# Performance work log

Hardware: AMD Instinct MI355X
Metric: run time of the kernel (lower is better)

Reference implementation:

```python
import jax, jax.numpy as jnp
import numpy as np

BLOCK = 32          # per_1x32 microscaling block size along K
FP4_MAX = 6.0       # largest magnitude representable in e2m1
FP4_EMAX = 2.0      # exponent of largest fp4 binade (4..6)


def _quant_dequant_mxfp4(x):
    """Simulate MXFP4 (e2m1 elements, shared power-of-two E8M0 scale per 1x32
    block along the last dim): quantize then dequantize. x: [..., K], K % 32 == 0."""
    shape = x.shape
    xb = x.reshape(*shape[:-1], shape[-1] // BLOCK, BLOCK)
    amax = jnp.max(jnp.abs(xb), axis=-1, keepdims=True)
    # shared scale: 2^(floor(log2(amax)) - emax) so the block max lands in the top binade
    exp = jnp.floor(jnp.log2(jnp.maximum(amax, jnp.finfo(x.dtype).tiny))) - FP4_EMAX
    scale = jnp.where(amax > 0, jnp.exp2(exp), jnp.ones_like(amax))
    q = jnp.clip(xb / scale, -FP4_MAX, FP4_MAX)
    aq = jnp.abs(q)
    # e2m1 ulp: 0.5 on [0,2), 1 on [2,4), 2 on [4,6]
    lsb = jnp.where(aq < 2.0, 0.5, jnp.where(aq < 4.0, 1.0, 2.0))
    qr = jnp.round(q / lsb) * lsb  # round-to-nearest-even onto the fp4 grid
    return (qr * scale).reshape(shape)


def setup_inputs() -> dict:
    key = jax.random.key(0)
    k1, k2, k3 = jax.random.split(key, 3)
    B, S, K, N = 4, 2048, 2048, 2048
    inp = jax.random.normal(k1, (B, S, K), dtype=jnp.float32)
    weight = jax.random.normal(k2, (N, K), dtype=jnp.float32) * (1.0 / np.sqrt(K))
    bias = jax.random.normal(k3, (N,), dtype=jnp.float32) * 0.02
    return {"input": inp, "weight": weight, "bias": bias}


def reference(input, weight, bias):
    # both activation and weight are fake-quantized to MXFP4 per 1x32 blocks
    # along the contraction (in_features) dim, then a standard GEMM + bias.
    orig_shape = input.shape
    a = _quant_dequant_mxfp4(input.reshape(-1, orig_shape[-1]))  # [M, K]
    w = _quant_dequant_mxfp4(weight)                              # [N, K]
    out = jnp.einsum("mk,nk->mn", a, w) + bias
    return out.reshape(*orig_shape[:-1], weight.shape[0])
```

## Files before the change

### kernel.cpp

```cpp
#include <hip/hip_runtime.h>
#include <cstdint>


#define BM 256
#define BN 256
#define BK 256

typedef float floatx16 __attribute__((ext_vector_type(16)));
typedef int intx8 __attribute__((ext_vector_type(8)));

#define GLOBAL_AS __attribute__((address_space(1)))
#define LDS_AS __attribute__((address_space(3)))


__device__ __forceinline__ int enc1(float x, float inv) {
    float q = x * inv;
    q = fminf(fmaxf(q, -6.0f), 6.0f);
    int s = (int)(__float_as_uint(q) >> 31) << 3;
    float aq = fabsf(q);
    float ilsb = aq < 2.0f ? 2.0f : (aq < 4.0f ? 1.0f : 0.5f);
    float lsb  = aq < 2.0f ? 0.5f : (aq < 4.0f ? 1.0f : 2.0f);
    float ar = rintf(aq * ilsb) * lsb;
    int c;
    if (ar < 2.0f)      c = (int)(ar * 2.0f);
    else if (ar < 4.0f) c = 2 + (int)ar;
    else                c = 4 + (int)(ar * 0.5f);
    return c | s;
}

__global__ void quant_mxfp4_v5(const float* __restrict__ A, uint8_t* __restrict__ Aq,
                               uint8_t* __restrict__ Asc,
                               const float* __restrict__ W, uint8_t* __restrict__ Wq,
                               uint8_t* __restrict__ Wsc,
                               long na4, long ntot4, int s4, long Mr, long Nr) {
    long t = (long)blockIdx.x * 256 + threadIdx.x;
    if (t >= ntot4) return;
    const float* src; uint8_t* dq; uint8_t* ds; long idx; long rows;
    if (t < na4) { src = A; dq = Aq; ds = Asc; idx = t; rows = Mr; }
    else         { src = W; dq = Wq; ds = Wsc; idx = t - na4; rows = Nr; }

    float4 f = ((const float4*)src)[idx];
    float amax = fmaxf(fmaxf(fabsf(f.x), fabsf(f.y)),
                       fmaxf(fabsf(f.z), fabsf(f.w)));
    amax = fmaxf(amax, __shfl_xor(amax, 1));
    amax = fmaxf(amax, __shfl_xor(amax, 2));
    amax = fmaxf(amax, __shfl_xor(amax, 4));

    int ebits = (int)((__float_as_uint(amax) >> 23) & 0xff);
    int sb;
    float inv;
    if (amax > 0.0f) {
        sb = ebits - 2; if (sb < 0) sb = 0;
        inv = __uint_as_float((unsigned)((256 - ebits) & 255) << 23);
    } else {
        sb = 127;
        inv = 0.0f;
    }

    int c0 = enc1(f.x, inv), c1 = enc1(f.y, inv);
    int c2 = enc1(f.z, inv), c3 = enc1(f.w, inv);
    ((unsigned short*)dq)[idx] =
        (unsigned short)(c0 | (c1 << 4) | (c2 << 8) | (c3 << 12));
    if ((idx & 7) == 0) {
        long m  = idx >> s4;
        int  kb = (int)((idx & ((1L << s4) - 1)) >> 3);
        ds[((size_t)(kb >> 3) * rows + m) * 8 + (kb & 7)] = (uint8_t)sb;
    }
}


#define GITER(T, CUR, NXT)                                                     \
  {                                                                            \
    const int p_ = (T) & 1;                                                    \
    const uint8_t* pa_ = sA[p_];                                               \
    const uint8_t* pb_ = sB[p_];                                               \
    if ((T) + 1 < NT) {                                                        \
      _Pragma("unroll") for (int mi = 0; mi < 4; ++mi)                         \
        sgA[NXT][mi] = *(const uint2*)(Asc +                                   \
            ((size_t)((T) + 1) * M + m0 + rA0 + mi * 32) * 8);                 \
      _Pragma("unroll") for (int ni = 0; ni < 2; ++ni)                         \
        sgB[NXT][ni] = *(const uint2*)(Wsc +                                   \
            ((size_t)((T) + 1) * N + n0 + rB0 + ni * 32) * 8);                 \
    }                                                                          \
    __builtin_amdgcn_sched_barrier(0);                                         \
    int4 fa_[4], fb_[2];                                                       \
    _Pragma("unroll") for (int mi = 0; mi < 4; ++mi)                           \
      fa_[mi] = *(const int4*)(pa_ + (rA0 + mi * 32) * 128 + (q2 ^ swz) * 16); \
    _Pragma("unroll") for (int ni = 0; ni < 2; ++ni)                           \
      fb_[ni] = *(const int4*)(pb_ + (rB0 + ni * 32) * 128 + (q2 ^ swz) * 16); \
    __builtin_amdgcn_s_setprio(1);                                             \
    _Pragma("unroll") for (int ks = 0; ks < 4; ++ks) {                         \
      int4 na_[4], nb_[2];                                                     \
      if (ks < 3) {                                                            \
        const int off_ = (((ks + 1) * 2 + q2) ^ swz) * 16;                     \
        _Pragma("unroll") for (int mi = 0; mi < 4; ++mi)                       \
          na_[mi] = *(const int4*)(pa_ + (rA0 + mi * 32) * 128 + off_);        \
        _Pragma("unroll") for (int ni = 0; ni < 2; ++ni)                       \
          nb_[ni] = *(const int4*)(pb_ + (rB0 + ni * 32) * 128 + off_);        \
      }                                                                        \
      int sav_[4], sbv_[2];                                                    \
      _Pragma("unroll") for (int mi = 0; mi < 4; ++mi)                         \
        sav_[mi] = (int)(((ks < 2) ? (sgA[CUR][mi].x >> ((ks * 2 + q2) * 8))   \
                   : (sgA[CUR][mi].y >> (((ks - 2) * 2 + q2) * 8))) & 0xffu);  \
      _Pragma("unroll") for (int ni = 0; ni < 2; ++ni)                         \
        sbv_[ni] = (int)(((ks < 2) ? (sgB[CUR][ni].x >> ((ks * 2 + q2) * 8))   \
                   : (sgB[CUR][ni].y >> (((ks - 2) * 2 + q2) * 8))) & 0xffu);  \
      intx8 b80_, b81_;                                                        \
      b80_[0] = fb_[0].x; b80_[1] = fb_[0].y; b80_[2] = fb_[0].z;              \
      b80_[3] = fb_[0].w; b80_[4] = 0; b80_[5] = 0; b80_[6] = 0; b80_[7] = 0;  \
      b81_[0] = fb_[1].x; b81_[1] = fb_[1].y; b81_[2] = fb_[1].z;              \
      b81_[3] = fb_[1].w; b81_[4] = 0; b81_[5] = 0; b81_[6] = 0; b81_[7] = 0;  \
      _Pragma("unroll") for (int mi = 0; mi < 4; ++mi) {                       \
        intx8 a8_;                                                             \
        a8_[0] = fa_[mi].x; a8_[1] = fa_[mi].y; a8_[2] = fa_[mi].z;            \
        a8_[3] = fa_[mi].w; a8_[4] = 0; a8_[5] = 0; a8_[6] = 0; a8_[7] = 0;    \
        acc[mi][0] = __builtin_amdgcn_mfma_scale_f32_32x32x64_f8f6f4(          \
            a8_, b80_, acc[mi][0], 4, 4, 0, sav_[mi], 0, sbv_[0]);             \
        acc[mi][1] = __builtin_amdgcn_mfma_scale_f32_32x32x64_f8f6f4(          \
            a8_, b81_, acc[mi][1], 4, 4, 0, sav_[mi], 0, sbv_[1]);             \
      }                                                                        \
      if (ks < 3) {                                                            \
        _Pragma("unroll") for (int mi = 0; mi < 4; ++mi) fa_[mi] = na_[mi];    \
        _Pragma("unroll") for (int ni = 0; ni < 2; ++ni) fb_[ni] = nb_[ni];    \
      }                                                                        \
    }                                                                          \
    __builtin_amdgcn_s_setprio(0);                                             \
    if ((T) + 1 < NT) {                                                        \
      asm volatile("s_waitcnt lgkmcnt(0)" ::: "memory");                       \
      __builtin_amdgcn_sched_barrier(0);                                       \
      __builtin_amdgcn_s_barrier();                                            \
      if ((T) + 2 < NT) stage((T) + 2);                                        \
      __builtin_amdgcn_sched_barrier(0);                                       \
      if ((T) + 2 < NT) asm volatile("s_waitcnt vmcnt(8)" ::: "memory");       \
      else              asm volatile("s_waitcnt vmcnt(0)" ::: "memory");       \
      __builtin_amdgcn_sched_barrier(0);                                       \
      __builtin_amdgcn_s_barrier();                                            \
    }                                                                          \
  }

__global__ __launch_bounds__(512, 2) void gemm_fp4_v9(
        const uint8_t* __restrict__ Aq, const uint8_t* __restrict__ Asc,
        const uint8_t* __restrict__ Wq, const uint8_t* __restrict__ Wsc,
        const float* __restrict__ bias, float* __restrict__ C,
        int M, int N, int K) {
    __shared__ __align__(16) uint8_t sA[2][BM * 128];
    __shared__ __align__(16) uint8_t sB[2][BN * 128];

    const int tid = threadIdx.x;
    const int lane = tid & 63;
    const int w = tid >> 6;
    const int wr = w >> 2;
    const int wc = w & 3;
    const int row32 = lane & 31;
    const int q2 = lane >> 5;

    const int id = blockIdx.x;
    const int g = id & 7, h = id >> 3;
    const int by = g * 4 + (h & 3);
    const int bx = h >> 2;
    const int m0 = by * BM;
    const int n0 = bx * BN;
    const int KB2 = K >> 1;
    const int NT = K / BK;

    const int rA0 = wr * 128 + row32;
    const int rB0 = wc * 64 + row32;
    const int swz = row32 & 7;

    floatx16 acc[4][2];
#pragma unroll
    for (int i = 0; i < 4; i++)
#pragma unroll
        for (int j = 0; j < 2; j++)
#pragma unroll
            for (int r = 0; r < 16; r++) acc[i][j][r] = 0.f;

    auto stage = [&](int tt) {
        const int bb = tt & 1;
        const int kb = tt * 128;
#pragma unroll
        for (int it = 0; it < 4; ++it) {
            int idx = it * 512 + tid;
            int row = idx >> 3, c = idx & 7;
            int gc = c ^ (row & 7);
            const uint8_t* src = Aq + (size_t)(m0 + row) * KB2 + kb + gc * 16;
            __builtin_amdgcn_global_load_lds((GLOBAL_AS void*)src,
                (LDS_AS void*)(&sA[bb][idx * 16]), 16, 0, 0);
        }
#pragma unroll
        for (int it = 0; it < 4; ++it) {
            int idx = it * 512 + tid;
            int row = idx >> 3, c = idx & 7;
            int gc = c ^ (row & 7);
            const uint8_t* src = Wq + (size_t)(n0 + row) * KB2 + kb + gc * 16;
            __builtin_amdgcn_global_load_lds((GLOBAL_AS void*)src,
                (LDS_AS void*)(&sB[bb][idx * 16]), 16, 0, 0);
        }
    };

    uint2 sgA[2][4], sgB[2][2];

    stage(0);
    __builtin_amdgcn_sched_barrier(0);
#pragma unroll
    for (int mi = 0; mi < 4; ++mi)
        sgA[0][mi] = *(const uint2*)(Asc + ((size_t)0 * M + m0 + rA0 + mi * 32) * 8);
#pragma unroll
    for (int ni = 0; ni < 2; ++ni)
        sgB[0][ni] = *(const uint2*)(Wsc + ((size_t)0 * N + n0 + rB0 + ni * 32) * 8);
    __builtin_amdgcn_sched_barrier(0);
    stage(1);
    __builtin_amdgcn_sched_barrier(0);
    asm volatile("s_waitcnt vmcnt(8)" ::: "memory");
    __builtin_amdgcn_sched_barrier(0);
    __builtin_amdgcn_s_barrier();

    for (int t = 0; t < NT; t += 2) {
        GITER(t, 0, 1);
        GITER(t + 1, 1, 0);
    }

#pragma unroll
    for (int ni = 0; ni < 2; ++ni) {
        int n = n0 + wc * 64 + ni * 32 + row32;
        float bv = bias[n];
#pragma unroll
        for (int mi = 0; mi < 4; ++mi) {
            int mb = m0 + wr * 128 + mi * 32 + 4 * q2;
#pragma unroll
            for (int r = 0; r < 16; ++r) {
                int m = mb + (r & 3) + 8 * (r >> 2);
                C[(size_t)m * N + n] = acc[mi][ni][r] + bv;
            }
        }
    }
}


extern "C" void kernel_launch(void* const* d_in, const int* in_sizes, int n_in,
                              void* d_out, int out_size, void* d_ws, size_t ws_size,
                              hipStream_t stream) {
    const float* inp  = (const float*)d_in[0];
    const float* wgt  = (const float*)d_in[1];
    const float* bias = (const float*)d_in[2];
    float* out = (float*)d_out;

    const int N = in_sizes[2];
    const int K = in_sizes[1] / N;
    const long M = (long)in_sizes[0] / K;

    uint8_t* Aq4 = (uint8_t*)d_ws;
    uint8_t* Wq4 = Aq4 + (size_t)M * K / 2;
    uint8_t* Asc = Wq4 + (size_t)N * K / 2;
    uint8_t* Wsc = Asc + (size_t)M * K / 32;

    int s4 = 0;
    while ((1 << s4) < (K >> 2)) ++s4;

    long na4   = (long)M * K / 4;
    long ntot4 = na4 + (long)N * K / 4;
    quant_mxfp4_v5<<<dim3((ntot4 + 255) / 256), dim3(256), 0, stream>>>(
        inp, Aq4, Asc, wgt, Wq4, Wsc, na4, ntot4, s4, M, (long)N);

    dim3 grid((N / BN) * (int)(M / BM));
    gemm_fp4_v9<<<grid, dim3(512), 0, stream>>>(
        Aq4, Asc, Wq4, Wsc, bias, out, (int)M, N, K);
}
```

Baseline: 188.2 us.

## Issue next-tile global-to-LDS staging before the final MFMA group

Restructures each K-tile iteration so the last k-slice's LDS fragments are read first. Then a single barrier is placed and the stage(T+2) global-to-LDS loads and next scale loads are issued before the final group of scaled MFMAs. This lets the async copies overlap with MFMA work instead of being issued after all compute. The explicit register double-buffering of LDS fragments across k-slices is dropped in favour of a plain load-then-MFMA sequence per slice, which may expose LDS latency. The tail wait is relaxed to vmcnt(6) to account for the reordered scale loads.

```diff
diff --git a/kernel.cpp b/kernel.cpp
--- a/kernel.cpp
+++ b/kernel.cpp
@@ -69,76 +69,79 @@
 }
 
 
+#define MFMAS(KS, CUR, FA, FB)                                                 \
+  {                                                                            \
+    int sav_[4], sbv_[2];                                                      \
+    _Pragma("unroll") for (int mi = 0; mi < 4; ++mi)                           \
+      sav_[mi] = (int)((((KS) < 2) ? (sgA[CUR][mi].x >> (((KS)*2 + q2)*8))     \
+                  : (sgA[CUR][mi].y >> ((((KS)-2)*2 + q2)*8))) & 0xffu);       \
+    _Pragma("unroll") for (int ni = 0; ni < 2; ++ni)                           \
+      sbv_[ni] = (int)((((KS) < 2) ? (sgB[CUR][ni].x >> (((KS)*2 + q2)*8))     \
+                  : (sgB[CUR][ni].y >> ((((KS)-2)*2 + q2)*8))) & 0xffu);       \
+    intx8 b80_, b81_;                                                          \
+    b80_[0] = FB[0].x; b80_[1] = FB[0].y; b80_[2] = FB[0].z;                   \
+    b80_[3] = FB[0].w; b80_[4] = 0; b80_[5] = 0; b80_[6] = 0; b80_[7] = 0;     \
+    b81_[0] = FB[1].x; b81_[1] = FB[1].y; b81_[2] = FB[1].z;                   \
+    b81_[3] = FB[1].w; b81_[4] = 0; b81_[5] = 0; b81_[6] = 0; b81_[7] = 0;     \
+    __builtin_amdgcn_s_setprio(1);                                             \
+    _Pragma("unroll") for (int mi = 0; mi < 4; ++mi) {                         \
+      intx8 a8_;                                                               \
+      a8_[0] = FA[mi].x; a8_[1] = FA[mi].y; a8_[2] = FA[mi].z;                 \
+      a8_[3] = FA[mi].w; a8_[4] = 0; a8_[5] = 0; a8_[6] = 0; a8_[7] = 0;       \
+      acc[mi][0] = __builtin_amdgcn_mfma_scale_f32_32x32x64_f8f6f4(            \
+          a8_, b80_, acc[mi][0], 4, 4, 0, sav_[mi], 0, sbv_[0]);               \
+      acc[mi][1] = __builtin_amdgcn_mfma_scale_f32_32x32x64_f8f6f4(            \
+          a8_, b81_, acc[mi][1], 4, 4, 0, sav_[mi], 0, sbv_[1]);               \
+    }                                                                          \
+    __builtin_amdgcn_s_setprio(0);                                             \
+  }
+
 #define GITER(T, CUR, NXT)                                                     \
   {                                                                            \
     const int p_ = (T) & 1;                                                    \
     const uint8_t* pa_ = sA[p_];                                               \
     const uint8_t* pb_ = sB[p_];                                               \
+    _Pragma("unroll") for (int ks = 0; ks < 3; ++ks) {                         \
+      int4 fa_[4], fb_[2];                                                     \
+      const int off_ = ((ks * 2 + q2) ^ swz) * 16;                             \
+      _Pragma("unroll") for (int mi = 0; mi < 4; ++mi)                         \
+        fa_[mi] = *(const int4*)(pa_ + (rA0 + mi * 32) * 128 + off_);          \
+      _Pragma("unroll") for (int ni = 0; ni < 2; ++ni)                         \
+        fb_[ni] = *(const int4*)(pb_ + (rB0 + ni * 32) * 128 + off_);          \
+      MFMAS(ks, CUR, fa_, fb_)                                                 \
+    }                                                                          \
+    int4 fa3_[4], fb3_[2];                                                     \
+    {                                                                          \
+      const int off_ = ((6 + q2) ^ swz) * 16;                                  \
+      _Pragma("unroll") for (int mi = 0; mi < 4; ++mi)                         \
+        fa3_[mi] = *(const int4*)(pa_ + (rA0 + mi * 32) * 128 + off_);         \
+      _Pragma("unroll") for (int ni = 0; ni < 2; ++ni)                         \
+        fb3_[ni] = *(const int4*)(pb_ + (rB0 + ni * 32) * 128 + off_);         \
+    }                                                                          \
     if ((T) + 1 < NT) {                                                        \
+      asm volatile("s_waitcnt lgkmcnt(0)" ::: "memory");                       \
+      __builtin_amdgcn_sched_barrier(0);                                       \
+      __builtin_amdgcn_s_barrier();        \
       _Pragma("unroll") for (int mi = 0; mi < 4; ++mi)                         \
         sgA[NXT][mi] = *(const uint2*)(Asc +                                   \
             ((size_t)((T) + 1) * M + m0 + rA0 + mi * 32) * 8);                 \
       _Pragma("unroll") for (int ni = 0; ni < 2; ++ni)                         \
         sgB[NXT][ni] = *(const uint2*)(Wsc +                                   \
             ((size_t)((T) + 1) * N + n0 + rB0 + ni * 32) * 8);                 \
-    }                                                                          \
-    __builtin_amdgcn_sched_barrier(0);                                         \
-    int4 fa_[4], fb_[2];                                                       \
-    _Pragma("unroll") for (int mi = 0; mi < 4; ++mi)                           \
-      fa_[mi] = *(const int4*)(pa_ + (rA0 + mi * 32) * 128 + (q2 ^ swz) * 16); \
-    _Pragma("unroll") for (int ni = 0; ni < 2; ++ni)                           \
-      fb_[ni] = *(const int4*)(pb_ + (rB0 + ni * 32) * 128 + (q2 ^ swz) * 16); \
-    __builtin_amdgcn_s_setprio(1);                                             \
-    _Pragma("unroll") for (int ks = 0; ks < 4; ++ks) {                         \
-      int4 na_[4], nb_[2];                                                     \
-      if (ks < 3) {                                                            \
-        const int off_ = (((ks + 1) * 2 + q2) ^ swz) * 16;                     \
-        _Pragma("unroll") for (int mi = 0; mi < 4; ++mi)                       \
-          na_[mi] = *(const int4*)(pa_ + (rA0 + mi * 32) * 128 + off_);        \
-        _Pragma("unroll") for (int ni = 0; ni < 2; ++ni)                       \
-          nb_[ni] = *(const int4*)(pb_ + (rB0 + ni * 32) * 128 + off_);        \
-      }                                                                        \
-      int sav_[4], sbv_[2];                                                    \
-      _Pragma("unroll") for (int mi = 0; mi < 4; ++mi)                         \
-        sav_[mi] = (int)(((ks < 2) ? (sgA[CUR][mi].x >> ((ks * 2 + q2) * 8))   \
-                   : (sgA[CUR][mi].y >> (((ks - 2) * 2 + q2) * 8))) & 0xffu);  \
-      _Pragma("unroll") for (int ni = 0; ni < 2; ++ni)                         \
-        sbv_[ni] = (int)(((ks < 2) ? (sgB[CUR][ni].x >> ((ks * 2 + q2) * 8))   \
-                   : (sgB[CUR][ni].y >> (((ks - 2) * 2 + q2) * 8))) & 0xffu);  \
-      intx8 b80_, b81_;                                                        \
-      b80_[0] = fb_[0].x; b80_[1] = fb_[0].y; b80_[2] = fb_[0].z;              \
-      b80_[3] = fb_[0].w; b80_[4] = 0; b80_[5] = 0; b80_[6] = 0; b80_[7] = 0;  \
-      b81_[0] = fb_[1].x; b81_[1] = fb_[1].y; b81_[2] = fb_[1].z;              \
-      b81_[3] = fb_[1].w; b81_[4] = 0; b81_[5] = 0; b81_[6] = 0; b81_[7] = 0;  \
-      _Pragma("unroll") for (int mi = 0; mi < 4; ++mi) {                       \
-        intx8 a8_;                                                             \
-        a8_[0] = fa_[mi].x; a8_[1] = fa_[mi].y; a8_[2] = fa_[mi].z;            \
-        a8_[3] = fa_[mi].w; a8_[4] = 0; a8_[5] = 0; a8_[6] = 0; a8_[7] = 0;    \
-        acc[mi][0] = __builtin_amdgcn_mfma_scale_f32_32x32x64_f8f6f4(          \
-            a8_, b80_, acc[mi][0], 4, 4, 0, sav_[mi], 0, sbv_[0]);             \
-        acc[mi][1] = __builtin_amdgcn_mfma_scale_f32_32x32x64_f8f6f4(          \
-            a8_, b81_, acc[mi][1], 4, 4, 0, sav_[mi], 0, sbv_[1]);             \
-      }                                                                        \
-      if (ks < 3) {                                                            \
-        _Pragma("unroll") for (int mi = 0; mi < 4; ++mi) fa_[mi] = na_[mi];    \
-        _Pragma("unroll") for (int ni = 0; ni < 2; ++ni) fb_[ni] = nb_[ni];    \
-      }                                                                        \
-    }                                                                          \
-    __builtin_amdgcn_s_setprio(0);                                             \
+      __builtin_amdgcn_sched_barrier(0);                                       \
+      if ((T) + 2 < NT) stage((T) + 2);                                        \
+      __builtin_amdgcn_sched_barrier(0);                                       \
+    }                                                                          \
+    MFMAS(3, CUR, fa3_, fb3_)                                                  \
     if ((T) + 1 < NT) {                                                        \
-      asm volatile("s_waitcnt lgkmcnt(0)" ::: "memory");                       \
-      __builtin_amdgcn_sched_barrier(0);                                       \
-      __builtin_amdgcn_s_barrier();                                            \
-      if ((T) + 2 < NT) stage((T) + 2);                                        \
-      __builtin_amdgcn_sched_barrier(0);                                       \
       if ((T) + 2 < NT) asm volatile("s_waitcnt vmcnt(8)" ::: "memory");       \
-      else              asm volatile("s_waitcnt vmcnt(0)" ::: "memory");       \
-      __builtin_amdgcn_sched_barrier(0);                                       \
-      __builtin_amdgcn_s_barrier();                                            \
+      else              asm volatile("s_waitcnt vmcnt(6)" ::: "memory");       \
+      __builtin_amdgcn_sched_barrier(0);                                       \
+      __builtin_amdgcn_s_barrier();                \
     }                                                                          \
   }
 
-__global__ __launch_bounds__(512, 2) void gemm_fp4_v9(
+__global__ __launch_bounds__(512, 2) void gemm_fp4_v10(
         const uint8_t* __restrict__ Aq, const uint8_t* __restrict__ Asc,
         const uint8_t* __restrict__ Wq, const uint8_t* __restrict__ Wsc,
         const float* __restrict__ bias, float* __restrict__ C,
@@ -204,10 +207,10 @@
     __builtin_amdgcn_sched_barrier(0);
 #pragma unroll
     for (int mi = 0; mi < 4; ++mi)
-        sgA[0][mi] = *(const uint2*)(Asc + ((size_t)0 * M + m0 + rA0 + mi * 32) * 8);
+        sgA[0][mi] = *(const uint2*)(Asc + ((size_t)m0 + rA0 + mi * 32) * 8);
 #pragma unroll
     for (int ni = 0; ni < 2; ++ni)
-        sgB[0][ni] = *(const uint2*)(Wsc + ((size_t)0 * N + n0 + rB0 + ni * 32) * 8);
+        sgB[0][ni] = *(const uint2*)(Wsc + ((size_t)n0 + rB0 + ni * 32) * 8);
     __builtin_amdgcn_sched_barrier(0);
     stage(1);
     __builtin_amdgcn_sched_barrier(0);
@@ -263,6 +266,6 @@
         inp, Aq4, Asc, wgt, Wq4, Wsc, na4, ntot4, s4, M, (long)N);
 
     dim3 grid((N / BN) * (int)(M / BM));
-    gemm_fp4_v9<<<grid, dim3(512), 0, stream>>>(
+    gemm_fp4_v10<<<grid, dim3(512), 0, stream>>>(
         Aq4, Asc, Wq4, Wsc, bias, out, (int)M, N, K);
 }
```

New measurement: 231.8 us. 1.23x slower.
